# Kernel optimization log

Hardware: AMD Instinct MI355X
Metric: run time of the kernel (lower is better)

Reference implementation:

```python
import jax, jax.numpy as jnp
import numpy as np

N, F, B = 4096, 2048, 2048


def setup_inputs() -> dict:
    key = jax.random.key(0)
    ks = jax.random.split(key, 11)
    s_h = 1.0 / np.sqrt(F).astype(np.float32)
    s_x = 1.0 / np.sqrt(B).astype(np.float32)
    inp = {
        "behavior": jax.random.normal(ks[0], (N, B), jnp.float32),
        "h0": jax.random.normal(ks[1], (N, F), jnp.float32),
        "c0": jax.random.normal(ks[2], (N, F), jnp.float32),
        "Wi_h": jax.random.normal(ks[3], (F, F), jnp.float32) * s_h,
        "Wi_x": jax.random.normal(ks[4], (B, F), jnp.float32) * s_x,
        "bi": jnp.zeros((F,), jnp.float32),
        "Wf_h": jax.random.normal(ks[5], (F, F), jnp.float32) * s_h,
        "Wf_x": jax.random.normal(ks[6], (B, F), jnp.float32) * s_x,
        "bf": jnp.zeros((F,), jnp.float32),
        "Wg_h": jax.random.normal(ks[7], (F, F), jnp.float32) * s_h,
        "Wg_x": jax.random.normal(ks[8], (B, F), jnp.float32) * s_x,
        "bg": jnp.zeros((F,), jnp.float32),
        "Wo_h": jax.random.normal(ks[9], (F, F), jnp.float32) * s_h,
        "Wo_x": jax.random.normal(ks[10], (B, F), jnp.float32) * s_x,
        "bo": jnp.zeros((F,), jnp.float32),
    }
    return inp


def reference(behavior, h0, c0, Wi_h, Wi_x, bi, Wf_h, Wf_x, bf,
              Wg_h, Wg_x, bg, Wo_h, Wo_x, bo):
    # Single-step LSTM cell: each gate is a two-input linear proj (h, behavior)
    def proj(Wh, Wx, b):
        return h0 @ Wh + behavior @ Wx + b  # [N, F]

    i = jax.nn.sigmoid(proj(Wi_h, Wi_x, bi))
    f = jax.nn.sigmoid(proj(Wf_h, Wf_x, bf))
    g = jnp.tanh(proj(Wg_h, Wg_x, bg))
    o = jax.nn.sigmoid(proj(Wo_h, Wo_x, bo))
    c = f * c0 + i * g
    h = o * jnp.tanh(c)
    return h
```

## Files before the change

kernel.cpp:

```cpp
#include <hip/hip_runtime.h>
#include <stdint.h>

#define N_ROWS 4096
#define F_DIM  2048
#define B_DIM  2048
#define K_DIM  4096

typedef __attribute__((ext_vector_type(8)))  __bf16 bf16x8;
typedef __attribute__((ext_vector_type(16))) float  f32x16;
typedef unsigned short u16;

__device__ __forceinline__ u16 f2bf(float x) {
  unsigned int u = __float_as_uint(x);
  u += 0x7fffu + ((u >> 16) & 1u);
  return (u16)(u >> 16);
}

__device__ __forceinline__ void async_copy16(const void* g, void* l) {
  __builtin_amdgcn_global_load_lds(
      (const __attribute__((address_space(1))) void*)g,
      (__attribute__((address_space(3))) void*)l, 16, 0, 0);
}

__device__ __forceinline__ float sigmoid_f(float x) {
  return 1.0f / (1.0f + __expf(-x));
}
__device__ __forceinline__ float tanh_f(float x) {
  float e2 = __expf(2.0f * x);
  return 1.0f - 2.0f / (e2 + 1.0f);
}

__global__ __launch_bounds__(256) void pack_x_kernel(
    const float* __restrict__ h0, const float* __restrict__ behavior,
    u16* __restrict__ Xc)
{
  int tid = blockIdx.x * 256 + threadIdx.x;
  int row = tid >> 9;
  int k0  = (tid & 511) * 8;
  const float* src = (k0 < F_DIM) ? (h0 + (size_t)row * F_DIM + k0)
                                  : (behavior + (size_t)row * B_DIM + (k0 - F_DIM));
  const float4* s4 = (const float4*)src;
  float4 a = s4[0], b = s4[1];
  uint4 o;
  o.x = (unsigned)f2bf(a.x) | ((unsigned)f2bf(a.y) << 16);
  o.y = (unsigned)f2bf(a.z) | ((unsigned)f2bf(a.w) << 16);
  o.z = (unsigned)f2bf(b.x) | ((unsigned)f2bf(b.y) << 16);
  o.w = (unsigned)f2bf(b.z) | ((unsigned)f2bf(b.w) << 16);
  *(uint4*)(Xc + (size_t)tid * 8) = o;
}

__global__ __launch_bounds__(256) void pack_w_kernel(
    const float* __restrict__ wi_h, const float* __restrict__ wi_x,
    const float* __restrict__ wf_h, const float* __restrict__ wf_x,
    const float* __restrict__ wg_h, const float* __restrict__ wg_x,
    const float* __restrict__ wo_h, const float* __restrict__ wo_x,
    u16* __restrict__ WT)
{
  __shared__ float tileT[32 * 65];
  int g = blockIdx.z;
  const float* Wh = (g == 0) ? wi_h : (g == 1) ? wf_h : (g == 2) ? wg_h : wo_h;
  const float* Wx = (g == 0) ? wi_x : (g == 1) ? wf_x : (g == 2) ? wg_x : wo_x;
  int fb = blockIdx.x * 32;
  int kb = blockIdx.y * 64;
  const float* W = (kb < F_DIM) ? Wh : Wx;
  int kofs = (kb < F_DIM) ? kb : (kb - F_DIM);

  int t  = threadIdx.x;
  int c4 = t & 7;
  int kr = t >> 3;
#pragma unroll
  for (int p = 0; p < 2; ++p) {
    int k_l = kr + p * 32;
    float4 v = *(const float4*)(W + (size_t)(kofs + k_l) * F_DIM + fb + c4 * 4);
    tileT[(c4 * 4 + 0) * 65 + k_l] = v.x;
    tileT[(c4 * 4 + 1) * 65 + k_l] = v.y;
    tileT[(c4 * 4 + 2) * 65 + k_l] = v.z;
    tileT[(c4 * 4 + 3) * 65 + k_l] = v.w;
  }
  __syncthreads();
  {
    int f_l = t >> 3;
    int k8  = (t & 7) * 8;
    const float* s = tileT + f_l * 65 + k8;
    uint4 o;
    o.x = (unsigned)f2bf(s[0]) | ((unsigned)f2bf(s[1]) << 16);
    o.y = (unsigned)f2bf(s[2]) | ((unsigned)f2bf(s[3]) << 16);
    o.z = (unsigned)f2bf(s[4]) | ((unsigned)f2bf(s[5]) << 16);
    o.w = (unsigned)f2bf(s[6]) | ((unsigned)f2bf(s[7]) << 16);
    *(uint4*)(WT + ((size_t)g * F_DIM + fb + f_l) * K_DIM + kb + k8) = o;
  }
}

__global__ __launch_bounds__(256, 2) void lstm_gemm_kernel(
    const u16* __restrict__ Xc, const u16* __restrict__ WT,
    const float* __restrict__ c0,
    const float* __restrict__ bi, const float* __restrict__ bff,
    const float* __restrict__ bg, const float* __restrict__ bo,
    float* __restrict__ out)
{
  __shared__ u16 As[128 * 64];
  __shared__ u16 Bs[4 * 64 * 64];

  const int tid  = threadIdx.x;
  const int lane = tid & 63;
  const int wv   = tid >> 6;
  const int bm   = blockIdx.x;
  const int bn   = blockIdx.y;

  const int rw = wv & 1;
  const int fh = wv >> 1;
  const int l31  = lane & 31;
  const int half = lane >> 5;

  const u16* agp[4];
  const u16* bgp[8];
#pragma unroll
  for (int j = 0; j < 4; ++j) {
    int c = j * 256 + tid;
    int r = c >> 3, o = (c & 7) ^ (r & 7);
    agp[j] = Xc + (size_t)(bm * 128 + r) * K_DIM + o * 8;
  }
#pragma unroll
  for (int g = 0; g < 4; ++g)
#pragma unroll
    for (int jj = 0; jj < 2; ++jj) {
      int c = jj * 256 + tid;
      int r = c >> 3, o = (c & 7) ^ (r & 7);
      bgp[g * 2 + jj] = WT + ((size_t)g * F_DIM + bn * 64 + r) * K_DIM + o * 8;
    }
  const unsigned ubase = (unsigned)(tid & ~63) * 16u;

  f32x16 acc[4][2];
#pragma unroll
  for (int g = 0; g < 4; ++g)
#pragma unroll
    for (int rh = 0; rh < 2; ++rh)
#pragma unroll
      for (int r = 0; r < 16; ++r) acc[g][rh][r] = 0.f;

  for (int kt = 0; kt < 64; ++kt) {
#pragma unroll
    for (int j = 0; j < 4; ++j)
      async_copy16(agp[j], (char*)As + j * 4096 + ubase);
#pragma unroll
    for (int j = 0; j < 8; ++j)
      async_copy16(bgp[j], (char*)Bs + (j >> 1) * 8192 + (j & 1) * 4096 + ubase);
#pragma unroll
    for (int j = 0; j < 4; ++j) agp[j] += 64;
#pragma unroll
    for (int j = 0; j < 8; ++j) bgp[j] += 64;
    __syncthreads();

#pragma unroll
    for (int c = 0; c < 4; ++c) {
      const int oct = c * 2 + half;
      const int sw  = oct ^ (l31 & 7);
      bf16x8 af[2];
#pragma unroll
      for (int rh = 0; rh < 2; ++rh) {
        int m = rw * 64 + rh * 32 + l31;
        af[rh] = *(const bf16x8*)(As + m * 64 + sw * 8);
      }
      bf16x8 bfr[4];
#pragma unroll
      for (int g = 0; g < 4; ++g) {
        int fl = fh * 32 + l31;
        bfr[g] = *(const bf16x8*)(Bs + g * 4096 + fl * 64 + sw * 8);
      }
#pragma unroll
      for (int g = 0; g < 4; ++g)
#pragma unroll
        for (int rh = 0; rh < 2; ++rh)
          acc[g][rh] = __builtin_amdgcn_mfma_f32_32x32x16_bf16(
              af[rh], bfr[g], acc[g][rh], 0, 0, 0);
    }
    __syncthreads();
  }

  {
    int f = bn * 64 + fh * 32 + l31;
    float b0 = bi[f], b1 = bff[f], b2 = bg[f], b3 = bo[f];
#pragma unroll
    for (int rh = 0; rh < 2; ++rh) {
      int row_base = bm * 128 + rw * 64 + rh * 32 + 4 * half;
#pragma unroll
      for (int r = 0; r < 16; ++r) {
        int row = row_base + (r & 3) + 8 * (r >> 2);
        size_t idx = (size_t)row * F_DIM + f;
        float pi = acc[0][rh][r] + b0;
        float pf = acc[1][rh][r] + b1;
        float pg = acc[2][rh][r] + b2;
        float po = acc[3][rh][r] + b3;
        float iv = sigmoid_f(pi);
        float fv = sigmoid_f(pf);
        float gv = tanh_f(pg);
        float ov = sigmoid_f(po);
        float cv = fv * c0[idx] + iv * gv;
        out[idx] = ov * tanh_f(cv);
      }
    }
  }
}

extern "C" void kernel_launch(void* const* d_in, const int* in_sizes, int n_in,
                              void* d_out, int out_size, void* d_ws, size_t ws_size,
                              hipStream_t stream) {
  const float* behavior = (const float*)d_in[0];
  const float* h0       = (const float*)d_in[1];
  const float* c0       = (const float*)d_in[2];
  const float* Wi_h     = (const float*)d_in[3];
  const float* Wi_x     = (const float*)d_in[4];
  const float* bi       = (const float*)d_in[5];
  const float* Wf_h     = (const float*)d_in[6];
  const float* Wf_x     = (const float*)d_in[7];
  const float* bf       = (const float*)d_in[8];
  const float* Wg_h     = (const float*)d_in[9];
  const float* Wg_x     = (const float*)d_in[10];
  const float* bg       = (const float*)d_in[11];
  const float* Wo_h     = (const float*)d_in[12];
  const float* Wo_x     = (const float*)d_in[13];
  const float* bo       = (const float*)d_in[14];
  float* out = (float*)d_out;

  u16* Xc = (u16*)d_ws;
  u16* WT = Xc + (size_t)N_ROWS * K_DIM;

  pack_x_kernel<<<dim3(N_ROWS * (K_DIM / 8) / 256), 256, 0, stream>>>(h0, behavior, Xc);
  pack_w_kernel<<<dim3(F_DIM / 32, K_DIM / 64, 4), 256, 0, stream>>>(
      Wi_h, Wi_x, Wf_h, Wf_x, Wg_h, Wg_x, Wo_h, Wo_x, WT);
  lstm_gemm_kernel<<<dim3(N_ROWS / 128, F_DIM / 64), 256, 0, stream>>>(
      Xc, WT, c0, bi, bf, bg, bo, out);
}
```

Before: 525.7 us.

## Double-buffer LDS with 512-thread 256-row tiles and split K-step prefetch

Raises the GEMM block to 512 threads covering 256 rows by 64 features across all four gates. The K step drops to 32 and uses a double-buffered 64KB LDS region, so the next tile loads asynchronously while the current one feeds MFMA. Explicit vmcnt waits and raw s_barrier replace __syncthreads, and MFMA issue runs under raised setprio. The larger tile raises operand reuse and the pipelining hides global latency, but LDS use per block doubles and occupancy may drop.

```diff
diff --git a/kernel.cpp b/kernel.cpp
--- a/kernel.cpp
+++ b/kernel.cpp
@@ -28,6 +28,10 @@
 __device__ __forceinline__ float tanh_f(float x) {
   float e2 = __expf(2.0f * x);
   return 1.0f - 2.0f / (e2 + 1.0f);
+}
+
+__device__ __forceinline__ f32x16 mm(bf16x8 a, bf16x8 b, f32x16 c) {
+  return __builtin_amdgcn_mfma_f32_32x32x16_bf16(a, b, c, 0, 0, 0);
 }
 
 __global__ __launch_bounds__(256) void pack_x_kernel(
@@ -91,15 +95,14 @@
   }
 }
 
-__global__ __launch_bounds__(256, 2) void lstm_gemm_kernel(
+__global__ __launch_bounds__(512, 2) void lstm_gemm_kernel(
     const u16* __restrict__ Xc, const u16* __restrict__ WT,
     const float* __restrict__ c0,
     const float* __restrict__ bi, const float* __restrict__ bff,
     const float* __restrict__ bg, const float* __restrict__ bo,
     float* __restrict__ out)
 {
-  __shared__ u16 As[128 * 64];
-  __shared__ u16 Bs[4 * 64 * 64];
+  __shared__ u16 Ls[32768];
 
   const int tid  = threadIdx.x;
   const int lane = tid & 63;
@@ -107,74 +110,105 @@
   const int bm   = blockIdx.x;
   const int bn   = blockIdx.y;
 
-  const int rw = wv & 1;
-  const int fh = wv >> 1;
+  const int rw   = wv & 3;
+  const int fh   = wv >> 2;
   const int l31  = lane & 31;
   const int half = lane >> 5;
-
-  const u16* agp[4];
-  const u16* bgp[8];
-#pragma unroll
-  for (int j = 0; j < 4; ++j) {
-    int c = j * 256 + tid;
-    int r = c >> 3, o = (c & 7) ^ (r & 7);
-    agp[j] = Xc + (size_t)(bm * 128 + r) * K_DIM + o * 8;
-  }
+  const int swb  = (l31 >> 1) & 3;
+
+  const u16* aSrc[2];
+  const u16* bSrc[2];
+#pragma unroll
+  for (int p = 0; p < 2; ++p) {
+    int c = p * 512 + tid;
+    int r = c >> 2, s = c & 3;
+    int o = s ^ ((r >> 1) & 3);
+    aSrc[p] = Xc + (size_t)(bm * 256 + r) * K_DIM + o * 8;
+    int g = c >> 8, cc = c & 255;
+    int rb = cc >> 2, sb2 = cc & 3;
+    int ob = sb2 ^ ((rb >> 1) & 3);
+    bSrc[p] = WT + ((size_t)g * F_DIM + bn * 64 + rb) * K_DIM + ob * 8;
+  }
+  const unsigned ub = (unsigned)(tid & ~63) * 16u;
+
+  f32x16 acc[4][2];
 #pragma unroll
   for (int g = 0; g < 4; ++g)
 #pragma unroll
-    for (int jj = 0; jj < 2; ++jj) {
-      int c = jj * 256 + tid;
-      int r = c >> 3, o = (c & 7) ^ (r & 7);
-      bgp[g * 2 + jj] = WT + ((size_t)g * F_DIM + bn * 64 + r) * K_DIM + o * 8;
-    }
-  const unsigned ubase = (unsigned)(tid & ~63) * 16u;
-
-  f32x16 acc[4][2];
-#pragma unroll
-  for (int g = 0; g < 4; ++g)
-#pragma unroll
     for (int rh = 0; rh < 2; ++rh)
 #pragma unroll
       for (int r = 0; r < 16; ++r) acc[g][rh][r] = 0.f;
 
-  for (int kt = 0; kt < 64; ++kt) {
-#pragma unroll
-    for (int j = 0; j < 4; ++j)
-      async_copy16(agp[j], (char*)As + j * 4096 + ubase);
-#pragma unroll
-    for (int j = 0; j < 8; ++j)
-      async_copy16(bgp[j], (char*)Bs + (j >> 1) * 8192 + (j & 1) * 4096 + ubase);
-#pragma unroll
-    for (int j = 0; j < 4; ++j) agp[j] += 64;
-#pragma unroll
-    for (int j = 0; j < 8; ++j) bgp[j] += 64;
-    __syncthreads();
-
-#pragma unroll
-    for (int c = 0; c < 4; ++c) {
-      const int oct = c * 2 + half;
-      const int sw  = oct ^ (l31 & 7);
-      bf16x8 af[2];
-#pragma unroll
-      for (int rh = 0; rh < 2; ++rh) {
-        int m = rw * 64 + rh * 32 + l31;
-        af[rh] = *(const bf16x8*)(As + m * 64 + sw * 8);
-      }
+#pragma unroll
+  for (int p = 0; p < 2; ++p) {
+    async_copy16(aSrc[p], (char*)Ls + p * 8192 + ub);
+    async_copy16(bSrc[p], (char*)Ls + 16384 + p * 8192 + ub);
+  }
+#pragma unroll
+  for (int p = 0; p < 2; ++p) { aSrc[p] += 32; bSrc[p] += 32; }
+
+  int cur = 0;
+  for (int kt = 0; kt < 128; ++kt) {
+    const int nb = cur ^ 1;
+    char* LdsN = (char*)Ls + nb * 32768;
+    const u16* Lb = Ls + cur * 16384;
+    const u16* Ab0 = Lb + (rw * 64 +      l31) * 32;
+    const u16* Ab1 = Lb + (rw * 64 + 32 + l31) * 32;
+    const u16* Bb  = Lb + 8192 + (fh * 32 + l31) * 32;
+
+    if (kt < 127) {
+      async_copy16(aSrc[0], LdsN + ub);
+      async_copy16(bSrc[0], LdsN + 16384 + ub);
+      asm volatile("s_waitcnt vmcnt(2)" ::: "memory");
+    } else {
+      asm volatile("s_waitcnt vmcnt(0)" ::: "memory");
+    }
+    __builtin_amdgcn_s_barrier();
+    {
+      const int sw8 = (half ^ swb) * 8;
+      bf16x8 af0 = *(const bf16x8*)(Ab0 + sw8);
+      bf16x8 af1 = *(const bf16x8*)(Ab1 + sw8);
       bf16x8 bfr[4];
 #pragma unroll
+      for (int g = 0; g < 4; ++g)
+        bfr[g] = *(const bf16x8*)(Bb + g * 2048 + sw8);
+      __builtin_amdgcn_s_setprio(1);
+#pragma unroll
       for (int g = 0; g < 4; ++g) {
-        int fl = fh * 32 + l31;
-        bfr[g] = *(const bf16x8*)(Bs + g * 4096 + fl * 64 + sw * 8);
-      }
+        acc[g][0] = mm(af0, bfr[g], acc[g][0]);
+        acc[g][1] = mm(af1, bfr[g], acc[g][1]);
+      }
+      __builtin_amdgcn_s_setprio(0);
+    }
+    __builtin_amdgcn_s_barrier();
+
+    {
+      const int sw8 = ((2 + half) ^ swb) * 8;
+      bf16x8 af0 = *(const bf16x8*)(Ab0 + sw8);
+      bf16x8 af1 = *(const bf16x8*)(Ab1 + sw8);
+      bf16x8 bfr[4];
 #pragma unroll
       for (int g = 0; g < 4; ++g)
-#pragma unroll
-        for (int rh = 0; rh < 2; ++rh)
-          acc[g][rh] = __builtin_amdgcn_mfma_f32_32x32x16_bf16(
-              af[rh], bfr[g], acc[g][rh], 0, 0, 0);
-    }
-    __syncthreads();
+        bfr[g] = *(const bf16x8*)(Bb + g * 2048 + sw8);
+      if (kt < 127) {
+        async_copy16(aSrc[1], LdsN + 8192 + ub);
+        async_copy16(bSrc[1], LdsN + 16384 + 8192 + ub);
+      }
+      __builtin_amdgcn_s_barrier();
+      __builtin_amdgcn_s_setprio(1);
+#pragma unroll
+      for (int g = 0; g < 4; ++g) {
+        acc[g][0] = mm(af0, bfr[g], acc[g][0]);
+        acc[g][1] = mm(af1, bfr[g], acc[g][1]);
+      }
+      __builtin_amdgcn_s_setprio(0);
+    }
+    asm volatile("s_waitcnt lgkmcnt(0)" ::: "memory");
+    __builtin_amdgcn_s_barrier();
+
+#pragma unroll
+    for (int p = 0; p < 2; ++p) { aSrc[p] += 32; bSrc[p] += 32; }
+    cur ^= 1;
   }
 
   {
@@ -182,7 +216,7 @@
     float b0 = bi[f], b1 = bff[f], b2 = bg[f], b3 = bo[f];
 #pragma unroll
     for (int rh = 0; rh < 2; ++rh) {
-      int row_base = bm * 128 + rw * 64 + rh * 32 + 4 * half;
+      int row_base = bm * 256 + rw * 64 + rh * 32 + 4 * half;
 #pragma unroll
       for (int r = 0; r < 16; ++r) {
         int row = row_base + (r & 3) + 8 * (r >> 2);
@@ -228,6 +262,6 @@
   pack_x_kernel<<<dim3(N_ROWS * (K_DIM / 8) / 256), 256, 0, stream>>>(h0, behavior, Xc);
   pack_w_kernel<<<dim3(F_DIM / 32, K_DIM / 64, 4), 256, 0, stream>>>(
       Wi_h, Wi_x, Wf_h, Wf_x, Wg_h, Wg_x, Wo_h, Wo_x, WT);
-  lstm_gemm_kernel<<<dim3(N_ROWS / 128, F_DIM / 64), 256, 0, stream>>>(
+  lstm_gemm_kernel<<<dim3(N_ROWS / 256, F_DIM / 64), 512, 0, stream>>>(
       Xc, WT, c0, bi, bf, bg, bo, out);
 }
```

Measured after the change: 536.0 us. Within noise of the previous version (+2.0%).
